# Optimization experiments

Measured on AMD Instinct MI355X. Metric: run time of the kernel, lower is better.

Reference implementation:

```python
import jax, jax.numpy as jnp
import numpy as np

N, C, DK, DV = 8192, 128, 64, 64


def setup_inputs() -> dict:
    key = jax.random.key(0)
    ks = jax.random.split(key, 7)
    x = jax.random.normal(ks[0], (N, C), dtype=jnp.float32)
    # kaiming_normal for weights (std = sqrt(2/fan_in)), torch-default uniform bias
    std = float(np.sqrt(2.0 / C))
    bb = float(1.0 / np.sqrt(C))
    Wq = jax.random.normal(ks[1], (DK, C), dtype=jnp.float32) * std
    Wk = jax.random.normal(ks[2], (DK, C), dtype=jnp.float32) * std
    Wv = jax.random.normal(ks[3], (DV, C), dtype=jnp.float32) * std
    bq = jax.random.uniform(ks[4], (DK,), dtype=jnp.float32, minval=-bb, maxval=bb)
    bk = jax.random.uniform(ks[5], (DK,), dtype=jnp.float32, minval=-bb, maxval=bb)
    bv = jax.random.uniform(ks[6], (DV,), dtype=jnp.float32, minval=-bb, maxval=bb)
    return {"polyline_feature": x, "Wq": Wq, "bq": bq, "Wk": Wk, "bk": bk, "Wv": Wv, "bv": bv}


def reference(polyline_feature, Wq, bq, Wk, bk, Wv, bv):
    x = polyline_feature
    Q = jax.nn.relu(x @ Wq.T + bq)  # [N, DK]
    K = jax.nn.relu(x @ Wk.T + bk)  # [N, DK]
    V = jax.nn.relu(x @ Wv.T + bv)  # [N, DV]
    scores = (Q @ K.T) / jnp.sqrt(jnp.asarray(K.shape[1], Q.dtype))  # [N, N]
    attn = jax.nn.softmax(scores, axis=1)
    return attn @ V + Q  # residual on Q (non-standard)
```

## Files before the change

kernel.cpp:

```cpp
#include <hip/hip_runtime.h>


typedef __attribute__((ext_vector_type(8))) __bf16 bf16x8;
typedef __attribute__((ext_vector_type(4))) float f32x4;
typedef __attribute__((ext_vector_type(16))) float f32x16;

constexpr int N_ROWS = 8192;
constexpr int CDIM   = 128;
constexpr int DKV    = 64;
constexpr float SCALE_Q = 0.125f * 1.4426950408889634f;

__device__ __forceinline__ float fast_exp2(float x) {
    return __builtin_amdgcn_exp2f(x);
}

__device__ __forceinline__ unsigned short f2bf(float x) {
    union { float f; unsigned u; } v; v.f = x;
    unsigned r = v.u + 0x7fffu + ((v.u >> 16) & 1u);
    return (unsigned short)(r >> 16);
}

union Frag {
    unsigned u32[4];
    unsigned short u16[8];
    bf16x8 b;
    f32x4 f;
};

__global__ __launch_bounds__(128) void qkv_kernel(
    const float* __restrict__ x,
    const float* __restrict__ Wq, const float* __restrict__ bq,
    const float* __restrict__ Wk, const float* __restrict__ bk,
    const float* __restrict__ Wv, const float* __restrict__ bv,
    unsigned short* __restrict__ Qb, unsigned short* __restrict__ Kb,
    unsigned short* __restrict__ Vt, float* __restrict__ Qf)
{
    const int tid = threadIdx.x;
    const int w  = tid >> 6;
    const int l  = tid & 63;
    const int g  = l >> 4;
    const int lm = l & 15;
    const int n_base = blockIdx.x * 32 + w * 16;

    bf16x8 af[4];
    {
        const float* xrow = x + (size_t)(n_base + lm) * CDIM;
        #pragma unroll
        for (int s = 0; s < 4; ++s) {
            f32x4 lo = *(const f32x4*)(xrow + s * 32 + g * 8);
            f32x4 hi = *(const f32x4*)(xrow + s * 32 + g * 8 + 4);
            Frag fr;
            #pragma unroll
            for (int j = 0; j < 4; ++j) { fr.u16[j] = f2bf(lo[j]); fr.u16[4 + j] = f2bf(hi[j]); }
            af[s] = fr.b;
        }
    }

    const float* Ws[3] = {Wq, Wk, Wv};
    const float* Bs[3] = {bq, bk, bv};
    #pragma unroll
    for (int mat = 0; mat < 3; ++mat) {
        #pragma unroll
        for (int ct = 0; ct < 4; ++ct) {
            const int f = ct * 16 + lm;
            const float* wrow = Ws[mat] + (size_t)f * CDIM;
            f32x4 acc = {0.f, 0.f, 0.f, 0.f};
            #pragma unroll
            for (int s = 0; s < 4; ++s) {
                f32x4 lo = *(const f32x4*)(wrow + s * 32 + g * 8);
                f32x4 hi = *(const f32x4*)(wrow + s * 32 + g * 8 + 4);
                Frag fr;
                #pragma unroll
                for (int j = 0; j < 4; ++j) { fr.u16[j] = f2bf(lo[j]); fr.u16[4 + j] = f2bf(hi[j]); }
                acc = __builtin_amdgcn_mfma_f32_16x16x32_bf16(af[s], fr.b, acc, 0, 0, 0);
            }
            const float bias = Bs[mat][f];
            #pragma unroll
            for (int j = 0; j < 4; ++j) {
                const int n = n_base + g * 4 + j;
                const float v = fmaxf(acc[j] + bias, 0.f);
                if (mat == 0) {
                    Qf[(size_t)n * DKV + f] = v;
                    Qb[(size_t)n * DKV + f] = f2bf(v * SCALE_Q);
                } else if (mat == 1) {
                    Kb[(size_t)n * DKV + f] = f2bf(v);
                } else {
                    Vt[(size_t)f * N_ROWS + n] = f2bf(v);
                }
            }
        }
    }
}

__global__ __launch_bounds__(256) void attn_kernel(
    const unsigned short* __restrict__ Qb, const unsigned short* __restrict__ Kb,
    const unsigned short* __restrict__ Vt,
    float* __restrict__ PartO, float* __restrict__ PartML,
    int kv_per_split)
{
    __shared__ __align__(16) unsigned short K_lds[2][64 * 64];
    __shared__ __align__(16) unsigned short V_lds[2][64 * 64];

    const int tid = threadIdx.x;
    const int w  = tid >> 6;
    const int l  = tid & 63;
    const int c  = l & 31;
    const int hB = l >> 5;
    const int qb = blockIdx.x;
    const int sp = blockIdx.y;
    const int q0 = qb * 128 + w * 32;
    const int kv0 = sp * kv_per_split;

    const int r0 = tid >> 3;
    const int c7 = tid & 7;
    const int sw = (c7 * 16) ^ ((r0 & 7) << 4);
    const int dst0 = r0 * 128 + sw;
    const int dst1 = (r0 + 32) * 128 + sw;

    f32x4 kreg0, kreg1, vreg0, vreg1;
#define STAGE_LOAD(T) do { \
    const unsigned short* ks_ = Kb + (size_t)(kv0 + (T) * 64 + r0) * DKV + c7 * 8; \
    kreg0 = *(const f32x4*)ks_; \
    kreg1 = *(const f32x4*)(ks_ + 32 * DKV); \
    const unsigned short* vs_ = Vt + (size_t)r0 * N_ROWS + kv0 + (T) * 64 + c7 * 8; \
    vreg0 = *(const f32x4*)vs_; \
    vreg1 = *(const f32x4*)(vs_ + 32 * N_ROWS); \
} while (0)
#define STAGE_WRITE(B) do { \
    *(f32x4*)((char*)&K_lds[B][0] + dst0) = kreg0; \
    *(f32x4*)((char*)&K_lds[B][0] + dst1) = kreg1; \
    *(f32x4*)((char*)&V_lds[B][0] + dst0) = vreg0; \
    *(f32x4*)((char*)&V_lds[B][0] + dst1) = vreg1; \
} while (0)

    bf16x8 qf0, qf1, qf2, qf3;
    {
        const unsigned short* qp = Qb + (size_t)(q0 + c) * DKV + hB * 8;
        qf0 = *(const bf16x8*)(qp);
        qf1 = *(const bf16x8*)(qp + 16);
        qf2 = *(const bf16x8*)(qp + 32);
        qf3 = *(const bf16x8*)(qp + 48);
    }

    f32x16 o0 = {}, o1 = {};
    float m = 0.f;
    float lsum = 0.f;

    const int nt = kv_per_split >> 6;
    STAGE_LOAD(0);
    STAGE_WRITE(0);
    if (nt > 1) STAGE_LOAD(1);
    __syncthreads();

    for (int t = 0; t < nt; ++t) {
        const char* Kl = (const char*)&K_lds[t & 1][0];
        const char* Vl = (const char*)&V_lds[t & 1][0];
        const int swz = (c & 7) << 4;

        f32x16 st0 = {}, st1 = {};
        #pragma unroll
        for (int ks = 0; ks < 4; ++ks) {
            const int cb = ks * 32 + hB * 16;
            bf16x8 a0 = *(const bf16x8*)(Kl + c * 128 + (cb ^ swz));
            bf16x8 a1 = *(const bf16x8*)(Kl + (32 + c) * 128 + (cb ^ swz));
            const bf16x8 qv = (ks == 0) ? qf0 : (ks == 1) ? qf1 : (ks == 2) ? qf2 : qf3;
            st0 = __builtin_amdgcn_mfma_f32_32x32x16_bf16(a0, qv, st0, 0, 0, 0);
            st1 = __builtin_amdgcn_mfma_f32_32x32x16_bf16(a1, qv, st1, 0, 0, 0);
        }

        float tmax = fmaxf(st0[0], st1[0]);
        #pragma unroll
        for (int r = 1; r < 16; ++r) tmax = fmaxf(tmax, fmaxf(st0[r], st1[r]));
        tmax = fmaxf(tmax, __shfl_xor(tmax, 32));

        if (!__all(tmax <= m + 8.f)) {
            const float mnew = fmaxf(m, tmax);
            const float alpha = fast_exp2(m - mnew);
            lsum *= alpha;
            #pragma unroll
            for (int r = 0; r < 16; ++r) { o0[r] *= alpha; o1[r] *= alpha; }
            m = mnew;
        }

        unsigned pk[16];
        float ls = 0.f;
        #pragma unroll
        for (int p = 0; p < 8; ++p) {
            float a = fast_exp2(st0[2 * p] - m);
            float b = fast_exp2(st0[2 * p + 1] - m);
            ls += a + b;
            union { unsigned u; __bf16 h[2]; } uu;
            uu.h[0] = (__bf16)a; uu.h[1] = (__bf16)b;
            pk[p] = uu.u;
        }
        #pragma unroll
        for (int p = 0; p < 8; ++p) {
            float a = fast_exp2(st1[2 * p] - m);
            float b = fast_exp2(st1[2 * p + 1] - m);
            ls += a + b;
            union { unsigned u; __bf16 h[2]; } uu;
            uu.h[0] = (__bf16)a; uu.h[1] = (__bf16)b;
            pk[8 + p] = uu.u;
        }
        lsum += ls;

        #pragma unroll
        for (int ks = 0; ks < 4; ++ks) {
            const int base = (ks >> 1) * 8 + (ks & 1) * 4;
            const unsigned ownA  = hB ? pk[base + 2] : pk[base + 0];
            const unsigned ownB  = hB ? pk[base + 3] : pk[base + 1];
            const unsigned contA = hB ? pk[base + 0] : pk[base + 2];
            const unsigned contB = hB ? pk[base + 1] : pk[base + 3];
            const unsigned crossA = __shfl_xor(contA, 32);
            const unsigned crossB = __shfl_xor(contB, 32);
            Frag pf;
            pf.u32[0] = hB ? crossA : ownA;
            pf.u32[1] = hB ? crossB : ownB;
            pf.u32[2] = hB ? ownA : crossA;
            pf.u32[3] = hB ? ownB : crossB;
            const int cb = ks * 32 + hB * 16;
            bf16x8 a0 = *(const bf16x8*)(Vl + c * 128 + (cb ^ swz));
            bf16x8 a1 = *(const bf16x8*)(Vl + (32 + c) * 128 + (cb ^ swz));
            o0 = __builtin_amdgcn_mfma_f32_32x32x16_bf16(a0, pf.b, o0, 0, 0, 0);
            o1 = __builtin_amdgcn_mfma_f32_32x32x16_bf16(a1, pf.b, o1, 0, 0, 0);
        }

        __syncthreads();
        if (t + 1 < nt) {
            STAGE_WRITE((t + 1) & 1);
            if (t + 2 < nt) STAGE_LOAD(t + 2);
            __syncthreads();
        }
    }
#undef STAGE_LOAD
#undef STAGE_WRITE

    lsum += __shfl_xor(lsum, 32);

    float* po = PartO + ((size_t)sp * N_ROWS + q0 + c) * 64;
    #pragma unroll
    for (int r = 0; r < 16; ++r) {
        const int dv = (r & 3) + 8 * (r >> 2) + 4 * hB;
        po[dv]      = o0[r];
        po[32 + dv] = o1[r];
    }
    if (hB == 0) {
        float* pml = PartML + ((size_t)sp * (N_ROWS / 32) + qb * 4 + w) * 64;
        pml[c]      = m;
        pml[32 + c] = lsum;
    }
}

__global__ __launch_bounds__(256) void merge_kernel(
    const float* __restrict__ PartO, const float* __restrict__ PartML,
    const float* __restrict__ Qf, float* __restrict__ out, int split)
{
    const int gid = blockIdx.x * 256 + threadIdx.x;
    const int q = gid >> 6;
    const int d = gid & 63;
    const int qt = q >> 5;
    const int qr = q & 31;

    float M = -1.0e30f;
    for (int s = 0; s < split; ++s)
        M = fmaxf(M, PartML[(size_t)(s * (N_ROWS / 32) + qt) * 64 + qr]);
    float L = 0.f;
    float acc = 0.f;
    for (int s = 0; s < split; ++s) {
        const float* pml = PartML + (size_t)(s * (N_ROWS / 32) + qt) * 64;
        const float wgt = fast_exp2(pml[qr] - M);
        L   += pml[32 + qr] * wgt;
        acc += PartO[((size_t)s * N_ROWS + q) * 64 + d] * wgt;
    }
    out[(size_t)q * 64 + d] = acc / L + Qf[(size_t)q * 64 + d];
}

extern "C" void kernel_launch(void* const* d_in, const int* in_sizes, int n_in,
                              void* d_out, int out_size, void* d_ws, size_t ws_size,
                              hipStream_t stream)
{
    const float* x  = (const float*)d_in[0];
    const float* Wq = (const float*)d_in[1];
    const float* bq = (const float*)d_in[2];
    const float* Wk = (const float*)d_in[3];
    const float* bk = (const float*)d_in[4];
    const float* Wv = (const float*)d_in[5];
    const float* bv = (const float*)d_in[6];
    float* out = (float*)d_out;

    char* ws = (char*)d_ws;
    size_t off = 0;
    auto take = [&](size_t bytes) {
        char* p = ws + off;
        off += (bytes + 255) & ~(size_t)255;
        return p;
    };
    unsigned short* Qb = (unsigned short*)take((size_t)N_ROWS * DKV * 2);
    unsigned short* Kb = (unsigned short*)take((size_t)N_ROWS * DKV * 2);
    unsigned short* Vt = (unsigned short*)take((size_t)DKV * N_ROWS * 2);
    float*          Qf = (float*)take((size_t)N_ROWS * DKV * 4);

    int split = 8;
    const size_t per_split = (size_t)N_ROWS * 64 * 4
                           + (size_t)(N_ROWS / 32) * 64 * 4 + 512;
    while (split > 1 && off + (size_t)split * per_split > ws_size) split >>= 1;

    float* PartO  = (float*)take((size_t)split * N_ROWS * 64 * 4);
    float* PartML = (float*)take((size_t)split * (N_ROWS / 32) * 64 * 4);

    qkv_kernel<<<dim3(N_ROWS / 32), dim3(128), 0, stream>>>(
        x, Wq, bq, Wk, bk, Wv, bv, Qb, Kb, Vt, Qf);
    attn_kernel<<<dim3(N_ROWS / 128, split), dim3(256), 0, stream>>>(
        Qb, Kb, Vt, PartO, PartML, N_ROWS / split);
    merge_kernel<<<dim3(N_ROWS * DKV / 256), dim3(256), 0, stream>>>(
        PartO, PartML, Qf, out, split);
}
```

Baseline: 56.51 us.

## Load K/V tiles directly into LDS and double the KV split count

Replaces the register-staged global-to-LDS copy of K and V tiles with direct global_load_lds transfers. The source column is XOR-swizzled so the existing LDS read pattern still holds. This drops the extra barrier and register traffic per iteration. It also raises the KV split from 8 to 16 and adds a min-blocks-per-CU launch bound of 4, to get more blocks in flight. The costs are more partial-result traffic for the merge kernel and a dependence on the barrier waiting for the async loads to finish.

```diff
diff --git a/kernel.cpp b/kernel.cpp
--- a/kernel.cpp
+++ b/kernel.cpp
@@ -92,7 +92,7 @@
     }
 }
 
-__global__ __launch_bounds__(256) void attn_kernel(
+__global__ __launch_bounds__(256, 4) void attn_kernel(
     const unsigned short* __restrict__ Qb, const unsigned short* __restrict__ Kb,
     const unsigned short* __restrict__ Vt,
     float* __restrict__ PartO, float* __restrict__ PartML,
@@ -111,26 +111,21 @@
     const int q0 = qb * 128 + w * 32;
     const int kv0 = sp * kv_per_split;
 
-    const int r0 = tid >> 3;
-    const int c7 = tid & 7;
-    const int sw = (c7 * 16) ^ ((r0 & 7) << 4);
-    const int dst0 = r0 * 128 + sw;
-    const int dst1 = (r0 + 32) * 128 + sw;
-
-    f32x4 kreg0, kreg1, vreg0, vreg1;
-#define STAGE_LOAD(T) do { \
-    const unsigned short* ks_ = Kb + (size_t)(kv0 + (T) * 64 + r0) * DKV + c7 * 8; \
-    kreg0 = *(const f32x4*)ks_; \
-    kreg1 = *(const f32x4*)(ks_ + 32 * DKV); \
-    const unsigned short* vs_ = Vt + (size_t)r0 * N_ROWS + kv0 + (T) * 64 + c7 * 8; \
-    vreg0 = *(const f32x4*)vs_; \
-    vreg1 = *(const f32x4*)(vs_ + 32 * N_ROWS); \
-} while (0)
-#define STAGE_WRITE(B) do { \
-    *(f32x4*)((char*)&K_lds[B][0] + dst0) = kreg0; \
-    *(f32x4*)((char*)&K_lds[B][0] + dst1) = kreg1; \
-    *(f32x4*)((char*)&V_lds[B][0] + dst0) = vreg0; \
-    *(f32x4*)((char*)&V_lds[B][0] + dst1) = vreg1; \
+    const int lrow = l >> 3;
+    const int srcc = ((l & 7) ^ lrow) * 8;
+
+#define ISSUE_LOADS(T, B) do { \
+    const int kvt_ = kv0 + (T) * 64; \
+    _Pragma("unroll") \
+    for (int i = 0; i < 2; ++i) { \
+        const int row_ = w * 16 + i * 8 + lrow; \
+        __builtin_amdgcn_global_load_lds( \
+            (const __attribute__((address_space(1))) unsigned int*)(Kb + (size_t)(kvt_ + row_) * DKV + srcc), \
+            (__attribute__((address_space(3))) unsigned int*)&K_lds[B][(w * 16 + i * 8) * 64], 16, 0, 0); \
+        __builtin_amdgcn_global_load_lds( \
+            (const __attribute__((address_space(1))) unsigned int*)(Vt + (size_t)row_ * N_ROWS + kvt_ + srcc), \
+            (__attribute__((address_space(3))) unsigned int*)&V_lds[B][(w * 16 + i * 8) * 64], 16, 0, 0); \
+    } \
 } while (0)
 
     bf16x8 qf0, qf1, qf2, qf3;
@@ -147,9 +142,8 @@
     float lsum = 0.f;
 
     const int nt = kv_per_split >> 6;
-    STAGE_LOAD(0);
-    STAGE_WRITE(0);
-    if (nt > 1) STAGE_LOAD(1);
+    ISSUE_LOADS(0, 0);
+    if (nt > 1) ISSUE_LOADS(1, 1);
     __syncthreads();
 
     for (int t = 0; t < nt; ++t) {
@@ -226,14 +220,9 @@
         }
 
         __syncthreads();
-        if (t + 1 < nt) {
-            STAGE_WRITE((t + 1) & 1);
-            if (t + 2 < nt) STAGE_LOAD(t + 2);
-            __syncthreads();
-        }
-    }
-#undef STAGE_LOAD
-#undef STAGE_WRITE
+        if (t + 2 < nt) ISSUE_LOADS(t + 2, t & 1);
+    }
+#undef ISSUE_LOADS
 
     lsum += __shfl_xor(lsum, 32);
 
@@ -300,7 +289,7 @@
     unsigned short* Vt = (unsigned short*)take((size_t)DKV * N_ROWS * 2);
     float*          Qf = (float*)take((size_t)N_ROWS * DKV * 4);
 
-    int split = 8;
+    int split = 16;
     const size_t per_split = (size_t)N_ROWS * 64 * 4
                            + (size_t)(N_ROWS / 32) * 64 * 4 + 512;
     while (split > 1 && off + (size_t)split * per_split > ws_size) split >>= 1;
```

After: 58.67 us. 3.8% more time.
